# Performance work log

Measured on AMD Instinct MI355X. Metric: run time of the kernel, lower is better.

## Reference

```python
import jax, jax.numpy as jnp
import numpy as np

N, D_IN, D_P, N_HEADS, N_CTRS, D_OUT = 8192, 256, 64, 8, 128, 256


def setup_inputs() -> dict:
    key = jax.random.key(0)
    k = jax.random.split(key, 6)
    x = jax.random.normal(k[0], (N, D_IN), dtype=jnp.float32)
    ctrs = jax.random.normal(k[1], (N_HEADS, N_CTRS, D_P), dtype=jnp.float32) * 0.5
    Wv = jax.random.normal(k[2], (N_HEADS, N_CTRS, D_P, D_P), dtype=jnp.float32) * 0.02
    Ov = jax.random.normal(k[3], (N_HEADS, N_CTRS, D_P), dtype=jnp.float32) * 0.02
    Wq = jax.random.normal(k[4], (D_IN, D_P, N_HEADS), dtype=jnp.float32) * 0.05
    Wo = jax.random.normal(k[5], (N_HEADS * D_P, D_OUT), dtype=jnp.float32) * 0.02
    return {"x": x, "ctrs": ctrs, "Wv": Wv, "Ov": Ov, "Wq": Wq, "Wo": Wo}


def reference(x, ctrs, Wv, Ov, Wq, Wo):
    # project input per head: (N,d_in) x (d_in,d_p,h) -> (h,N,d_p)
    x_in = jnp.einsum('ni,iph->hnp', x, Wq)
    # RBF soft assignments over centroids: (h,N,c)
    dist_sq = jnp.sum((x_in[:, :, None, :] - ctrs[:, None, :, :]) ** 2, axis=-1)
    assignments = jax.nn.softmax(-dist_sq, axis=2)
    # soft-weighted per-cluster matrices: (h,N,g,p)
    scored_weights = jnp.einsum('hnc,hcgp->hngp', assignments, Wv)
    # soft-weighted offsets: (h,N,p)
    scored_offsets = jnp.einsum('hnc,hcp->hnp', assignments, Ov)
    # elementwise multiply (broadcast over g) then reduce over g, as in original
    heads_out = jnp.sum(scored_weights * x_in[:, :, None, :], axis=2) + scored_offsets
    # NOTE: original reshapes (h,N,p) directly into (N, h*p) in row-major order
    heads_out = heads_out.reshape(x.shape[0], N_HEADS * D_P)
    return heads_out @ Wo
```

## Files before the change

kernel.cpp:

```cpp
#include <hip/hip_runtime.h>
#include <math.h>

#define NROWS 8192
#define DIN   256
#define NH    8
#define NC    128
#define DOUT  256

typedef unsigned short ushort_t;
typedef __attribute__((ext_vector_type(8))) short bf16x8;
typedef __attribute__((ext_vector_type(4))) float f32x4;
typedef __attribute__((ext_vector_type(8))) unsigned short u16x8;

static __device__ __forceinline__ ushort_t f2bf(float f) {
  union { float f; unsigned u; } v; v.f = f;
  unsigned r = v.u + 0x7fffu + ((v.u >> 16) & 1u);
  return (ushort_t)(r >> 16);
}
static __device__ __forceinline__ float bf2f(ushort_t h) {
  union { unsigned u; float f; } v; v.u = ((unsigned)h) << 16;
  return v.f;
}

#define MFMA16(a, b, c) __builtin_amdgcn_mfma_f32_16x16x32_bf16((a), (b), (c), 0, 0, 0)
#define GLOAD_LDS16(g, l)                                                     \
  __builtin_amdgcn_global_load_lds(                                           \
      (const __attribute__((address_space(1))) void*)(g),                     \
      (__attribute__((address_space(3))) void*)(l), 16, 0, 0)

__global__ __launch_bounds__(256) void prep_kernel(
    const float* __restrict__ Wq, const float* __restrict__ ctrs,
    const float* __restrict__ Wo, const float* __restrict__ Wv,
    const float* __restrict__ Ov, ushort_t* __restrict__ wcvtT,
    ushort_t* __restrict__ ctr3T, float* __restrict__ cbias,
    ushort_t* __restrict__ WoT, ushort_t* __restrict__ W2bT) {
  int bid = blockIdx.x;
  int t = threadIdx.x;
  if (bid < 512) {
    int j = bid, k = t;
    int h = j >> 6, p = j & 63;
    float v = Wq[((size_t)k * 64 + p) * 8 + h];
    ushort_t hi = f2bf(v), lo = f2bf(v - bf2f(hi));
    wcvtT[(size_t)j * 512 + k]       = hi;
    wcvtT[(size_t)j * 512 + 256 + k] = lo;
  } else if (bid < 768) {
    int idx = (bid - 512) * 4 + (t >> 6);
    int p = t & 63;
    float v = ctrs[(size_t)idx * 64 + p];
    float sq = v * v;
    #pragma unroll
    for (int off = 32; off >= 1; off >>= 1) sq += __shfl_xor(sq, off, 64);
    if (p == 0) cbias[idx] = -sq;
    ushort_t hi = f2bf(v), lo = f2bf(v - bf2f(hi));
    ctr3T[(size_t)idx * 192 + p]       = hi;
    ctr3T[(size_t)idx * 192 + 64 + p]  = lo;
    ctr3T[(size_t)idx * 192 + 128 + p] = hi;
  } else if (bid < 1280) {
    int k = bid - 768;
    int n = t;
    WoT[(size_t)n * 512 + k] = f2bf(Wo[(size_t)k * 256 + n]);
  } else {
    int b = (bid - 1280) * 4 + (t >> 6);
    int p = t & 63;
    int h = b >> 7, c = b & 127;
    const float* wv = Wv + (size_t)b * 4096;
    float acc = 0.f;
    #pragma unroll 16
    for (int g = 0; g < 64; ++g) acc += wv[g * 64 + p];
    W2bT[((size_t)h * 128 + p) * 128 + c]      = f2bf(acc);
    W2bT[((size_t)h * 128 + 64 + p) * 128 + c] = f2bf(Ov[(size_t)b * 64 + p]);
  }
}

__global__ __launch_bounds__(256) void gemm2_kernel(
    const ushort_t* __restrict__ A, const ushort_t* __restrict__ Bt,
    float* __restrict__ out) {
  __shared__ ushort_t At[32 * 64];
  __shared__ ushort_t Bl[64 * 64];
  const int t = threadIdx.x;
  const int w = t >> 6, l = t & 63;
  const int wr = w >> 1, wc = w & 1;
  const int m0 = (blockIdx.x >> 2) * 32, n0 = (blockIdx.x & 3) * 64;
  const int lr = l & 15, lk = l >> 4;

  f32x4 acc[2];
  #pragma unroll
  for (int b = 0; b < 2; ++b) acc[b] = (f32x4){0.f, 0.f, 0.f, 0.f};

  for (int k0 = 0; k0 < 512; k0 += 64) {
    {
      int q = w * 64 + l;
      int row = q >> 3, s = q & 7;
      int kl = k0 + ((s ^ (row & 7)) << 3);
      GLOAD_LDS16(A + (size_t)(m0 + row) * 512 + kl,
                  (char*)At + (size_t)w * 1024);
    }
    #pragma unroll
    for (int i = 0; i < 2; ++i) {
      int q = (i * 4 + w) * 64 + l;
      int row = q >> 3, s = q & 7;
      int kl = k0 + ((s ^ (row & 7)) << 3);
      GLOAD_LDS16(Bt + (size_t)(n0 + row) * 512 + kl,
                  (char*)Bl + (size_t)(i * 4 + w) * 1024);
    }
    __syncthreads();
    #pragma unroll
    for (int kk = 0; kk < 2; ++kk) {
      int rowa = wr * 16 + lr;
      int sa = (kk * 4 + lk) ^ (rowa & 7);
      bf16x8 af = *(const bf16x8*)((const char*)At + rowa * 128 + sa * 16);
      #pragma unroll
      for (int b = 0; b < 2; ++b) {
        int row = wc * 32 + b * 16 + lr;
        int s = (kk * 4 + lk) ^ (row & 7);
        bf16x8 bfr = *(const bf16x8*)((const char*)Bl + row * 128 + s * 16);
        acc[b] = MFMA16(af, bfr, acc[b]);
      }
    }
    __syncthreads();
  }
  #pragma unroll
  for (int b = 0; b < 2; ++b) {
    #pragma unroll
    for (int r = 0; r < 4; ++r) {
      int rowg = m0 + wr * 16 + lk * 4 + r;
      int colg = n0 + wc * 32 + b * 16 + lr;
      out[(size_t)rowg * 256 + colg] = acc[b][r];
    }
  }
}

__global__ __launch_bounds__(512, 4) void fused_pair_kernel(
    const float* __restrict__ x,
    const ushort_t* __restrict__ wcvtT,
    const ushort_t* __restrict__ ctr3T,
    const float* __restrict__ cbias,
    const ushort_t* __restrict__ W2bT,
    ushort_t* __restrict__ ho2) {
  __shared__ __align__(16) char Au_raw[36864];
  __shared__ char B0lds[16384];
  __shared__ char B1lds[16384];
  __shared__ float cb_lds[128];

  ushort_t* Axh = (ushort_t*)Au_raw;
  ushort_t* Axl = (ushort_t*)(Au_raw + 18432);
  ushort_t* A1  = (ushort_t*)Au_raw;
  ushort_t* A2  = (ushort_t*)Au_raw;

  const int t = threadIdx.x;
  const int w = t >> 6, l = t & 63;
  const int lr = l & 15, lk = l >> 4;
  const int h = blockIdx.x >> 6;
  const int n0 = (blockIdx.x & 63) * 128;

#define STAGE_B(BUF, SRC, LDB, KOFF)                                          \
  {                                                                           \
    _Pragma("unroll")                                                         \
    for (int i = 0; i < 2; ++i) {                                             \
      int q = (i * 8 + w) * 64 + l;                                           \
      int row = q >> 3, s = q & 7;                                            \
      GLOAD_LDS16((SRC) + (size_t)(h * 128 + row) * (LDB) + (KOFF) +          \
                      ((s ^ (row & 7)) << 3),                                 \
                  (char*)(BUF) + (size_t)(i * 8 + w) * 1024);                 \
    }                                                                         \
  }

#define STAGE_BX(BUF, KC)                                                     \
  {                                                                           \
    _Pragma("unroll")                                                         \
    for (int i = 0; i < 2; ++i) {                                             \
      int q = (i * 8 + w) * 64 + l;                                           \
      int row = q >> 3, s = q & 7;                                            \
      int sw = (s ^ (row & 7)) << 3;                                          \
      int jj = h * 64 + (row & 63);                                           \
      int koff = (row < 64 ? 0 : 256) + (KC) * 64 + sw;                       \
      GLOAD_LDS16(wcvtT + (size_t)jj * 512 + koff,                            \
                  (char*)(BUF) + (size_t)(i * 8 + w) * 1024);                 \
    }                                                                         \
  }

#define MFMA_STEP(BUF, ACC, KBASE, ASPLIT)                                    \
  {                                                                           \
    _Pragma("unroll")                                                         \
    for (int kk = 0; kk < 2; ++kk) {                                          \
      int klog = (KBASE) + kk * 32 + lk * 8;                                  \
      int kp = (ASPLIT) ? (klog < 64 ? klog : klog - 64) : klog;              \
      bf16x8 af = *(const bf16x8*)&A1[(w * 16 + lr) * 136 + kp];              \
      _Pragma("unroll")                                                       \
      for (int cj = 0; cj < 8; ++cj) {                                        \
        int brow = cj * 16 + lr;                                              \
        int slot = (kk * 4 + lk) ^ (brow & 7);                                \
        bf16x8 bfr =                                                          \
            *(const bf16x8*)((const char*)(BUF) + brow * 128 + slot * 16);    \
        (ACC)[cj] = MFMA16(af, bfr, (ACC)[cj]);                               \
      }                                                                       \
    }                                                                         \
  }

#define MFMAX(BUF)                                                            \
  {                                                                           \
    _Pragma("unroll")                                                         \
    for (int kk = 0; kk < 2; ++kk) {                                          \
      bf16x8 ah = *(const bf16x8*)&Axh[(w * 16 + lr) * 72 + kk * 32 + lk * 8];\
      bf16x8 al = *(const bf16x8*)&Axl[(w * 16 + lr) * 72 + kk * 32 + lk * 8];\
      _Pragma("unroll")                                                       \
      for (int cj = 0; cj < 4; ++cj) {                                        \
        int rh = cj * 16 + lr;                                                \
        int slot = (kk * 4 + lk) ^ (rh & 7);                                  \
        bf16x8 bh = *(const bf16x8*)((const char*)(BUF) + rh * 128 + slot * 16);\
        bf16x8 bl = *(const bf16x8*)((const char*)(BUF) + (64 + rh) * 128 + slot * 16);\
        acc_x[cj] = MFMA16(ah, bh, acc_x[cj]);                                \
        acc_x[cj] = MFMA16(al, bh, acc_x[cj]);                                \
        acc_x[cj] = MFMA16(ah, bl, acc_x[cj]);                                \
      }                                                                       \
    }                                                                         \
  }

#define BAR() __builtin_amdgcn_s_barrier()
#define SCHED() __builtin_amdgcn_sched_barrier(0)
#define WAITALL_BAR()                                                         \
  {                                                                           \
    asm volatile("s_waitcnt vmcnt(0) lgkmcnt(0)" ::: "memory");               \
    SCHED(); BAR(); SCHED();                                                  \
  }

  const int xrow = t >> 2;
  const int xseg = (t & 3) << 4;
  const float* xb = x + (size_t)(n0 + xrow) * 256 + xseg;
  float4 xr[4];

#define LOAD_X(KC)                                                            \
  {                                                                           \
    _Pragma("unroll")                                                         \
    for (int j = 0; j < 4; ++j) xr[j] = *(const float4*)(xb + (KC) * 64 + j * 4); \
  }

#define CVT_AX()                                                              \
  {                                                                           \
    u16x8 hv0, hv1, lv0, lv1;                                                 \
    _Pragma("unroll")                                                         \
    for (int j = 0; j < 2; ++j) {                                             \
      float f4[8] = {xr[j*2].x, xr[j*2].y, xr[j*2].z, xr[j*2].w,              \
                     xr[j*2+1].x, xr[j*2+1].y, xr[j*2+1].z, xr[j*2+1].w};     \
      _Pragma("unroll")                                                       \
      for (int e = 0; e < 8; ++e) {                                           \
        ushort_t hi = f2bf(f4[e]);                                            \
        if (j == 0) { hv0[e] = hi; lv0[e] = f2bf(f4[e] - bf2f(hi)); }         \
        else        { hv1[e] = hi; lv1[e] = f2bf(f4[e] - bf2f(hi)); }         \
      }                                                                       \
    }                                                                         \
    *(u16x8*)&Axh[xrow * 72 + xseg]     = hv0;                                \
    *(u16x8*)&Axh[xrow * 72 + xseg + 8] = hv1;                                \
    *(u16x8*)&Axl[xrow * 72 + xseg]     = lv0;                                \
    *(u16x8*)&Axl[xrow * 72 + xseg + 8] = lv1;                                \
  }

#define SOFTMAX(ACC)                                                          \
  {                                                                           \
    float cbv[8];                                                             \
    _Pragma("unroll")                                                         \
    for (int cj = 0; cj < 8; ++cj) cbv[cj] = cb_lds[cj * 16 + lr];            \
    _Pragma("unroll")                                                         \
    for (int r = 0; r < 4; ++r) {                                             \
      float v[8];                                                             \
      float m = -1e30f;                                                       \
      _Pragma("unroll")                                                       \
      for (int cj = 0; cj < 8; ++cj) {                                        \
        v[cj] = 2.f * (ACC)[cj][r] + cbv[cj];                                 \
        m = fmaxf(m, v[cj]);                                                  \
      }                                                                       \
      m = fmaxf(m, __shfl_xor(m, 1, 64));                                     \
      m = fmaxf(m, __shfl_xor(m, 2, 64));                                     \
      m = fmaxf(m, __shfl_xor(m, 4, 64));                                     \
      m = fmaxf(m, __shfl_xor(m, 8, 64));                                     \
      float s = 0.f;                                                          \
      _Pragma("unroll")                                                       \
      for (int cj = 0; cj < 8; ++cj) {                                        \
        v[cj] = __expf(v[cj] - m);                                            \
        s += v[cj];                                                           \
      }                                                                       \
      s += __shfl_xor(s, 1, 64);                                              \
      s += __shfl_xor(s, 2, 64);                                              \
      s += __shfl_xor(s, 4, 64);                                              \
      s += __shfl_xor(s, 8, 64);                                              \
      float inv = 1.f / s;                                                    \
      int row = w * 16 + lk * 4 + r;                                          \
      _Pragma("unroll")                                                       \
      for (int cj = 0; cj < 8; ++cj)                                          \
        A2[row * 136 + cj * 16 + lr] = f2bf(v[cj] * inv);                     \
    }                                                                         \
  }

  cb_lds[t & 127] = cbias[h * 128 + (t & 127)];
  STAGE_BX(B0lds, 0);
  LOAD_X(0);
  f32x4 acc_x[4];
  #pragma unroll
  for (int cj = 0; cj < 4; ++cj) acc_x[cj] = (f32x4){0.f, 0.f, 0.f, 0.f};
  CVT_AX();
  WAITALL_BAR();

  STAGE_BX(B1lds, 1);
  LOAD_X(1);
  MFMAX(B0lds);
  CVT_AX();
  WAITALL_BAR();
  STAGE_BX(B0lds, 2);
  LOAD_X(2);
  MFMAX(B1lds);
  CVT_AX();
  WAITALL_BAR();
  STAGE_BX(B1lds, 3);
  LOAD_X(3);
  MFMAX(B0lds);
  CVT_AX();
  WAITALL_BAR();
  STAGE_B(B0lds, ctr3T, 192, 0);
  MFMAX(B1lds);
  WAITALL_BAR();

  STAGE_B(B1lds, ctr3T, 192, 64);
  #pragma unroll
  for (int cj = 0; cj < 4; ++cj) {
    #pragma unroll
    for (int r = 0; r < 4; ++r) {
      int row = w * 16 + lk * 4 + r;
      int p = cj * 16 + lr;
      float v0 = acc_x[cj][r];
      ushort_t hi0 = f2bf(v0);
      A1[row * 136 + p] = hi0;
      A1[row * 136 + 64 + p] = f2bf(v0 - bf2f(hi0));
    }
  }
  f32x4 acc[8];
  #pragma unroll
  for (int cj = 0; cj < 8; ++cj) acc[cj] = (f32x4){0.f, 0.f, 0.f, 0.f};
  MFMA_STEP(B0lds, acc, 0, 1);
  WAITALL_BAR();
  STAGE_B(B0lds, ctr3T, 192, 128);
  MFMA_STEP(B1lds, acc, 64, 1);
  WAITALL_BAR();
  STAGE_B(B1lds, W2bT, 128, 0);
  MFMA_STEP(B0lds, acc, 128, 1);
  WAITALL_BAR();
  STAGE_B(B0lds, W2bT, 128, 64);
  SOFTMAX(acc);
  f32x4 accT[8];
  #pragma unroll
  for (int cj = 0; cj < 8; ++cj) accT[cj] = (f32x4){0.f, 0.f, 0.f, 0.f};
  MFMA_STEP(B1lds, accT, 0, 0);
  WAITALL_BAR();
  MFMA_STEP(B0lds, accT, 64, 0);
  #pragma unroll
  for (int cj = 0; cj < 4; ++cj) {
    #pragma unroll
    for (int r = 0; r < 4; ++r) {
      int row = w * 16 + lk * 4 + r;
      int p = cj * 16 + lr;
      float hov = acc_x[cj][r] * accT[cj][r] + accT[cj + 4][r];
      ((ushort_t*)B1lds)[row * 64 + p] = f2bf(hov);
    }
  }
  asm volatile("s_waitcnt lgkmcnt(0)" ::: "memory");
  SCHED(); BAR(); SCHED();
  #pragma unroll
  for (int i = 0; i < 2; ++i) {
    int q = i * 512 + t;
    int row = q >> 3, s = q & 7;
    uint4 v = *(const uint4*)((const char*)B1lds + row * 128 + s * 16);
    *(uint4*)(ho2 + ((size_t)h * NROWS + n0 + row) * 64 + s * 8) = v;
  }
#undef STAGE_B
#undef STAGE_BX
#undef MFMA_STEP
#undef MFMAX
#undef BAR
#undef SCHED
#undef WAITALL_BAR
#undef LOAD_X
#undef CVT_AX
#undef SOFTMAX
}

extern "C" void kernel_launch(void* const* d_in, const int* in_sizes, int n_in,
                              void* d_out, int out_size, void* d_ws, size_t ws_size,
                              hipStream_t stream) {
  (void)in_sizes; (void)n_in; (void)out_size; (void)ws_size;
  const float* x    = (const float*)d_in[0];
  const float* ctrs = (const float*)d_in[1];
  const float* Wv   = (const float*)d_in[2];
  const float* Ov   = (const float*)d_in[3];
  const float* Wq   = (const float*)d_in[4];
  const float* Wo   = (const float*)d_in[5];
  float* out = (float*)d_out;

  char* wsb = (char*)d_ws;
  ushort_t* wcvtT = (ushort_t*)wsb;
  ushort_t* ctr3T = (ushort_t*)(wsb + 524288);
  float*    cb    = (float*)   (wsb + 917504);
  ushort_t* W2bT  = (ushort_t*)(wsb + 921600);
  ushort_t* WoT   = (ushort_t*)(wsb + 1183744);
  ushort_t* ho2   = (ushort_t*)(wsb + 2097152);

  prep_kernel<<<1536, 256, 0, stream>>>(Wq, ctrs, Wo, Wv, Ov,
                                        wcvtT, ctr3T, cb, WoT, W2bT);
  fused_pair_kernel<<<512, 512, 0, stream>>>(x, wcvtT, ctr3T, cb, W2bT, ho2);
  gemm2_kernel<<<1024, 256, 0, stream>>>(ho2, WoT, out);
}
```

Measured before the change: 39.86 us.

## Replace split-bf16 emulation with single fp16 MFMA for projection and distance GEMMs

The x·Wq projection and the x_in·ctrs distance GEMM used to emulate higher precision with bf16 hi/lo splits, costing three MFMAs per product and doubling staged bytes. Both now use a single fp16 MFMA on fp16-converted operands. The K-loop is restaged in 128-wide chunks, which removes two pipeline stages and their barriers. Prep writes smaller fp16 workspaces. The trade-off is lower accuracy in the softmax logits, where fp16 rounding of x and of the projected features gets amplified, and overflow is possible if values exceed the fp16 range.

```diff
diff --git a/kernel.cpp b/kernel.cpp
--- a/kernel.cpp
+++ b/kernel.cpp
@@ -9,8 +9,8 @@
 
 typedef unsigned short ushort_t;
 typedef __attribute__((ext_vector_type(8))) short bf16x8;
+typedef __attribute__((ext_vector_type(8))) _Float16 f16x8;
 typedef __attribute__((ext_vector_type(4))) float f32x4;
-typedef __attribute__((ext_vector_type(8))) unsigned short u16x8;
 
 static __device__ __forceinline__ ushort_t f2bf(float f) {
   union { float f; unsigned u; } v; v.f = f;
@@ -23,6 +23,7 @@
 }
 
 #define MFMA16(a, b, c) __builtin_amdgcn_mfma_f32_16x16x32_bf16((a), (b), (c), 0, 0, 0)
+#define MFMA16F(a, b, c) __builtin_amdgcn_mfma_f32_16x16x32_f16((a), (b), (c), 0, 0, 0)
 #define GLOAD_LDS16(g, l)                                                     \
   __builtin_amdgcn_global_load_lds(                                           \
       (const __attribute__((address_space(1))) void*)(g),                     \
@@ -31,8 +32,8 @@
 __global__ __launch_bounds__(256) void prep_kernel(
     const float* __restrict__ Wq, const float* __restrict__ ctrs,
     const float* __restrict__ Wo, const float* __restrict__ Wv,
-    const float* __restrict__ Ov, ushort_t* __restrict__ wcvtT,
-    ushort_t* __restrict__ ctr3T, float* __restrict__ cbias,
+    const float* __restrict__ Ov, _Float16* __restrict__ wq16,
+    _Float16* __restrict__ ctr16, float* __restrict__ cbias,
     ushort_t* __restrict__ WoT, ushort_t* __restrict__ W2bT) {
   int bid = blockIdx.x;
   int t = threadIdx.x;
@@ -40,9 +41,7 @@
     int j = bid, k = t;
     int h = j >> 6, p = j & 63;
     float v = Wq[((size_t)k * 64 + p) * 8 + h];
-    ushort_t hi = f2bf(v), lo = f2bf(v - bf2f(hi));
-    wcvtT[(size_t)j * 512 + k]       = hi;
-    wcvtT[(size_t)j * 512 + 256 + k] = lo;
+    wq16[(size_t)j * 256 + k] = (_Float16)v;
   } else if (bid < 768) {
     int idx = (bid - 512) * 4 + (t >> 6);
     int p = t & 63;
@@ -51,10 +50,7 @@
     #pragma unroll
     for (int off = 32; off >= 1; off >>= 1) sq += __shfl_xor(sq, off, 64);
     if (p == 0) cbias[idx] = -sq;
-    ushort_t hi = f2bf(v), lo = f2bf(v - bf2f(hi));
-    ctr3T[(size_t)idx * 192 + p]       = hi;
-    ctr3T[(size_t)idx * 192 + 64 + p]  = lo;
-    ctr3T[(size_t)idx * 192 + 128 + p] = hi;
+    ctr16[(size_t)idx * 64 + p] = (_Float16)v;
   } else if (bid < 1280) {
     int k = bid - 768;
     int n = t;
@@ -132,19 +128,18 @@
 
 __global__ __launch_bounds__(512, 4) void fused_pair_kernel(
     const float* __restrict__ x,
-    const ushort_t* __restrict__ wcvtT,
-    const ushort_t* __restrict__ ctr3T,
+    const _Float16* __restrict__ wq16,
+    const _Float16* __restrict__ ctr16,
     const float* __restrict__ cbias,
     const ushort_t* __restrict__ W2bT,
     ushort_t* __restrict__ ho2) {
-  __shared__ __align__(16) char Au_raw[36864];
+  __shared__ __align__(16) char Au_raw[34816];
   __shared__ char B0lds[16384];
   __shared__ char B1lds[16384];
   __shared__ float cb_lds[128];
 
-  ushort_t* Axh = (ushort_t*)Au_raw;
-  ushort_t* Axl = (ushort_t*)(Au_raw + 18432);
-  ushort_t* A1  = (ushort_t*)Au_raw;
+  _Float16* Axf = (_Float16*)Au_raw;
+  _Float16* A1f = (_Float16*)Au_raw;
   ushort_t* A2  = (ushort_t*)Au_raw;
 
   const int t = threadIdx.x;
@@ -153,39 +148,73 @@
   const int h = blockIdx.x >> 6;
   const int n0 = (blockIdx.x & 63) * 128;
 
-#define STAGE_B(BUF, SRC, LDB, KOFF)                                          \
+#define STAGE_WQ2(BUF, KC2)                                                   \
   {                                                                           \
     _Pragma("unroll")                                                         \
     for (int i = 0; i < 2; ++i) {                                             \
-      int q = (i * 8 + w) * 64 + l;                                           \
+      int q = (i * 8 + w) * 64 + l;                              \
+      int jrow = q >> 4, s16 = q & 15;                                        \
+      int c2 = s16 >> 3, s = s16 & 7;                                         \
+      GLOAD_LDS16(wq16 + (size_t)(h * 64 + jrow) * 256 + (KC2) * 128 +        \
+                      c2 * 64 + ((s ^ (jrow & 7)) << 3),                      \
+                  (char*)(BUF) + (size_t)q * 16);                             \
+    }                                                                         \
+  }
+
+#define STAGE_B128(BUF, SRC, LDB, KOFF)                                       \
+  {                                                                           \
+    _Pragma("unroll")                                                         \
+    for (int i = 0; i < 2; ++i) {                                             \
+      int q = (i * 8 + w) * 64 + l;                              \
       int row = q >> 3, s = q & 7;                                            \
       GLOAD_LDS16((SRC) + (size_t)(h * 128 + row) * (LDB) + (KOFF) +          \
                       ((s ^ (row & 7)) << 3),                                 \
-                  (char*)(BUF) + (size_t)(i * 8 + w) * 1024);                 \
-    }                                                                         \
-  }
-
-#define STAGE_BX(BUF, KC)                                                     \
-  {                                                                           \
-    _Pragma("unroll")                                                         \
-    for (int i = 0; i < 2; ++i) {                                             \
-      int q = (i * 8 + w) * 64 + l;                                           \
-      int row = q >> 3, s = q & 7;                                            \
-      int sw = (s ^ (row & 7)) << 3;                                          \
-      int jj = h * 64 + (row & 63);                                           \
-      int koff = (row < 64 ? 0 : 256) + (KC) * 64 + sw;                       \
-      GLOAD_LDS16(wcvtT + (size_t)jj * 512 + koff,                            \
-                  (char*)(BUF) + (size_t)(i * 8 + w) * 1024);                 \
-    }                                                                         \
-  }
-
-#define MFMA_STEP(BUF, ACC, KBASE, ASPLIT)                                    \
+                  (char*)(BUF) + (size_t)q * 16);                             \
+    }                                                                         \
+  }
+
+#define MFMAX(BUF)                                                            \
+  {                                                                           \
+    _Pragma("unroll")                                                         \
+    for (int c2 = 0; c2 < 2; ++c2) {                                          \
+      _Pragma("unroll")                                                       \
+      for (int kk = 0; kk < 2; ++kk) {                                        \
+        f16x8 af = *(const f16x8*)&Axf[(w * 16 + lr) * 136 + c2 * 64 +        \
+                                       kk * 32 + lk * 8];                     \
+        _Pragma("unroll")                                                     \
+        for (int cj = 0; cj < 4; ++cj) {                                      \
+          int rh = cj * 16 + lr;                                              \
+          int slot = (kk * 4 + lk) ^ (rh & 7);                                \
+          f16x8 bfr = *(const f16x8*)((const char*)(BUF) + rh * 256 +         \
+                                      c2 * 128 + slot * 16);                  \
+          acc_x[cj] = MFMA16F(af, bfr, acc_x[cj]);                            \
+        }                                                                     \
+      }                                                                       \
+    }                                                                         \
+  }
+
+#define MFMA_L(BUF, ACC)                                                      \
   {                                                                           \
     _Pragma("unroll")                                                         \
     for (int kk = 0; kk < 2; ++kk) {                                          \
-      int klog = (KBASE) + kk * 32 + lk * 8;                                  \
-      int kp = (ASPLIT) ? (klog < 64 ? klog : klog - 64) : klog;              \
-      bf16x8 af = *(const bf16x8*)&A1[(w * 16 + lr) * 136 + kp];              \
+      f16x8 af = *(const f16x8*)&A1f[(w * 16 + lr) * 136 + kk * 32 + lk * 8]; \
+      _Pragma("unroll")                                                       \
+      for (int cj = 0; cj < 8; ++cj) {                                        \
+        int brow = cj * 16 + lr;                                              \
+        int slot = (kk * 4 + lk) ^ (brow & 7);                                \
+        f16x8 bfr =                                                           \
+            *(const f16x8*)((const char*)(BUF) + brow * 128 + slot * 16);     \
+        (ACC)[cj] = MFMA16F(af, bfr, (ACC)[cj]);                              \
+      }                                                                       \
+    }                                                                         \
+  }
+
+#define MFMA_T(BUF, ACC, KB)                                                  \
+  {                                                                           \
+    _Pragma("unroll")                                                         \
+    for (int kk = 0; kk < 2; ++kk) {                                          \
+      bf16x8 af = *(const bf16x8*)&A2[(w * 16 + lr) * 136 + (KB) + kk * 32 +  \
+                                      lk * 8];                                \
       _Pragma("unroll")                                                       \
       for (int cj = 0; cj < 8; ++cj) {                                        \
         int brow = cj * 16 + lr;                                              \
@@ -197,25 +226,6 @@
     }                                                                         \
   }
 
-#define MFMAX(BUF)                                                            \
-  {                                                                           \
-    _Pragma("unroll")                                                         \
-    for (int kk = 0; kk < 2; ++kk) {                                          \
-      bf16x8 ah = *(const bf16x8*)&Axh[(w * 16 + lr) * 72 + kk * 32 + lk * 8];\
-      bf16x8 al = *(const bf16x8*)&Axl[(w * 16 + lr) * 72 + kk * 32 + lk * 8];\
-      _Pragma("unroll")                                                       \
-      for (int cj = 0; cj < 4; ++cj) {                                        \
-        int rh = cj * 16 + lr;                                                \
-        int slot = (kk * 4 + lk) ^ (rh & 7);                                  \
-        bf16x8 bh = *(const bf16x8*)((const char*)(BUF) + rh * 128 + slot * 16);\
-        bf16x8 bl = *(const bf16x8*)((const char*)(BUF) + (64 + rh) * 128 + slot * 16);\
-        acc_x[cj] = MFMA16(ah, bh, acc_x[cj]);                                \
-        acc_x[cj] = MFMA16(al, bh, acc_x[cj]);                                \
-        acc_x[cj] = MFMA16(ah, bl, acc_x[cj]);                                \
-      }                                                                       \
-    }                                                                         \
-  }
-
 #define BAR() __builtin_amdgcn_s_barrier()
 #define SCHED() __builtin_amdgcn_sched_barrier(0)
 #define WAITALL_BAR()                                                         \
@@ -225,132 +235,109 @@
   }
 
   const int xrow = t >> 2;
-  const int xseg = (t & 3) << 4;
-  const float* xb = x + (size_t)(n0 + xrow) * 256 + xseg;
-  float4 xr[4];
-
-#define LOAD_X(KC)                                                            \
-  {                                                                           \
-    _Pragma("unroll")                                                         \
-    for (int j = 0; j < 4; ++j) xr[j] = *(const float4*)(xb + (KC) * 64 + j * 4); \
-  }
-
-#define CVT_AX()                                                              \
-  {                                                                           \
-    u16x8 hv0, hv1, lv0, lv1;                                                 \
-    _Pragma("unroll")                                                         \
-    for (int j = 0; j < 2; ++j) {                                             \
-      float f4[8] = {xr[j*2].x, xr[j*2].y, xr[j*2].z, xr[j*2].w,              \
-                     xr[j*2+1].x, xr[j*2+1].y, xr[j*2+1].z, xr[j*2+1].w};     \
-      _Pragma("unroll")                                                       \
-      for (int e = 0; e < 8; ++e) {                                           \
-        ushort_t hi = f2bf(f4[e]);                                            \
-        if (j == 0) { hv0[e] = hi; lv0[e] = f2bf(f4[e] - bf2f(hi)); }         \
-        else        { hv1[e] = hi; lv1[e] = f2bf(f4[e] - bf2f(hi)); }         \
-      }                                                                       \
-    }                                                                         \
-    *(u16x8*)&Axh[xrow * 72 + xseg]     = hv0;                                \
-    *(u16x8*)&Axh[xrow * 72 + xseg + 8] = hv1;                                \
-    *(u16x8*)&Axl[xrow * 72 + xseg]     = lv0;                                \
-    *(u16x8*)&Axl[xrow * 72 + xseg + 8] = lv1;                                \
-  }
-
-#define SOFTMAX(ACC)                                                          \
-  {                                                                           \
-    float cbv[8];                                                             \
-    _Pragma("unroll")                                                         \
-    for (int cj = 0; cj < 8; ++cj) cbv[cj] = cb_lds[cj * 16 + lr];            \
-    _Pragma("unroll")                                                         \
-    for (int r = 0; r < 4; ++r) {                                             \
-      float v[8];                                                             \
-      float m = -1e30f;                                                       \
-      _Pragma("unroll")                                                       \
-      for (int cj = 0; cj < 8; ++cj) {                                        \
-        v[cj] = 2.f * (ACC)[cj][r] + cbv[cj];                                 \
-        m = fmaxf(m, v[cj]);                                                  \
-      }                                                                       \
-      m = fmaxf(m, __shfl_xor(m, 1, 64));                                     \
-      m = fmaxf(m, __shfl_xor(m, 2, 64));                                     \
-      m = fmaxf(m, __shfl_xor(m, 4, 64));                                     \
-      m = fmaxf(m, __shfl_xor(m, 8, 64));                                     \
-      float s = 0.f;                                                          \
-      _Pragma("unroll")                                                       \
-      for (int cj = 0; cj < 8; ++cj) {                                        \
-        v[cj] = __expf(v[cj] - m);                                            \
-        s += v[cj];                                                           \
-      }                                                                       \
-      s += __shfl_xor(s, 1, 64);                                              \
-      s += __shfl_xor(s, 2, 64);                                              \
-      s += __shfl_xor(s, 4, 64);                                              \
-      s += __shfl_xor(s, 8, 64);                                              \
-      float inv = 1.f / s;                                                    \
-      int row = w * 16 + lk * 4 + r;                                          \
-      _Pragma("unroll")                                                       \
-      for (int cj = 0; cj < 8; ++cj)                                          \
-        A2[row * 136 + cj * 16 + lr] = f2bf(v[cj] * inv);                     \
+  const int xsegf = (t & 3) << 4;
+  const float* xb = x + (size_t)(n0 + xrow) * 256 + xsegf;
+  float4 xr[8];
+
+#define LOAD_X2(KC2)                                                          \
+  {                                                                           \
+    _Pragma("unroll")                                                         \
+    for (int c2 = 0; c2 < 2; ++c2)                                            \
+      _Pragma("unroll")                                                       \
+      for (int j = 0; j < 4; ++j)                                             \
+        xr[c2 * 4 + j] =                                                      \
+            *(const float4*)(xb + (KC2) * 128 + c2 * 64 + j * 4);             \
+  }
+
+#define CVT_AX2()                                                             \
+  {                                                                           \
+    _Pragma("unroll")                                                         \
+    for (int c2 = 0; c2 < 2; ++c2) {                                          \
+      f16x8 h0, h1;                                                           \
+      float f0[8] = {xr[c2*4].x,   xr[c2*4].y,   xr[c2*4].z,   xr[c2*4].w,    \
+                     xr[c2*4+1].x, xr[c2*4+1].y, xr[c2*4+1].z, xr[c2*4+1].w}; \
+      float f1[8] = {xr[c2*4+2].x, xr[c2*4+2].y, xr[c2*4+2].z, xr[c2*4+2].w,  \
+                     xr[c2*4+3].x, xr[c2*4+3].y, xr[c2*4+3].z, xr[c2*4+3].w}; \
+      _Pragma("unroll")                                                       \
+      for (int e = 0; e < 8; ++e) { h0[e] = (_Float16)f0[e];                  \
+                                    h1[e] = (_Float16)f1[e]; }                \
+      *(f16x8*)&Axf[xrow * 136 + c2 * 64 + xsegf]     = h0;                   \
+      *(f16x8*)&Axf[xrow * 136 + c2 * 64 + xsegf + 8] = h1;                   \
     }                                                                         \
   }
 
   cb_lds[t & 127] = cbias[h * 128 + (t & 127)];
-  STAGE_BX(B0lds, 0);
-  LOAD_X(0);
+  STAGE_WQ2(B0lds, 0);
+  LOAD_X2(0);
   f32x4 acc_x[4];
   #pragma unroll
   for (int cj = 0; cj < 4; ++cj) acc_x[cj] = (f32x4){0.f, 0.f, 0.f, 0.f};
-  CVT_AX();
-  WAITALL_BAR();
-
-  STAGE_BX(B1lds, 1);
-  LOAD_X(1);
+  CVT_AX2();
+  WAITALL_BAR();
+
+  STAGE_WQ2(B1lds, 1);
+  LOAD_X2(1);
   MFMAX(B0lds);
-  CVT_AX();
-  WAITALL_BAR();
-  STAGE_BX(B0lds, 2);
-  LOAD_X(2);
+  CVT_AX2();
+  WAITALL_BAR();
+  STAGE_B128(B0lds, ctr16, 64, 0);
   MFMAX(B1lds);
-  CVT_AX();
-  WAITALL_BAR();
-  STAGE_BX(B1lds, 3);
-  LOAD_X(3);
-  MFMAX(B0lds);
-  CVT_AX();
-  WAITALL_BAR();
-  STAGE_B(B0lds, ctr3T, 192, 0);
-  MFMAX(B1lds);
-  WAITALL_BAR();
-
-  STAGE_B(B1lds, ctr3T, 192, 64);
   #pragma unroll
   for (int cj = 0; cj < 4; ++cj) {
     #pragma unroll
     for (int r = 0; r < 4; ++r) {
       int row = w * 16 + lk * 4 + r;
-      int p = cj * 16 + lr;
-      float v0 = acc_x[cj][r];
-      ushort_t hi0 = f2bf(v0);
-      A1[row * 136 + p] = hi0;
-      A1[row * 136 + 64 + p] = f2bf(v0 - bf2f(hi0));
-    }
-  }
+      A1f[row * 136 + cj * 16 + lr] = (_Float16)acc_x[cj][r];
+    }
+  }
+  WAITALL_BAR();
+  STAGE_B128(B1lds, W2bT, 128, 0);
   f32x4 acc[8];
   #pragma unroll
   for (int cj = 0; cj < 8; ++cj) acc[cj] = (f32x4){0.f, 0.f, 0.f, 0.f};
-  MFMA_STEP(B0lds, acc, 0, 1);
-  WAITALL_BAR();
-  STAGE_B(B0lds, ctr3T, 192, 128);
-  MFMA_STEP(B1lds, acc, 64, 1);
-  WAITALL_BAR();
-  STAGE_B(B1lds, W2bT, 128, 0);
-  MFMA_STEP(B0lds, acc, 128, 1);
-  WAITALL_BAR();
-  STAGE_B(B0lds, W2bT, 128, 64);
-  SOFTMAX(acc);
+  MFMA_L(B0lds, acc);
+  {
+    float cbv[8];
+    #pragma unroll
+    for (int cj = 0; cj < 8; ++cj) cbv[cj] = cb_lds[cj * 16 + lr];
+    #pragma unroll
+    for (int r = 0; r < 4; ++r) {
+      float v[8];
+      float m = -1e30f;
+      #pragma unroll
+      for (int cj = 0; cj < 8; ++cj) {
+        v[cj] = 2.f * acc[cj][r] + cbv[cj];
+        m = fmaxf(m, v[cj]);
+      }
+      m = fmaxf(m, __shfl_xor(m, 1, 64));
+      m = fmaxf(m, __shfl_xor(m, 2, 64));
+      m = fmaxf(m, __shfl_xor(m, 4, 64));
+      m = fmaxf(m, __shfl_xor(m, 8, 64));
+      float s = 0.f;
+      #pragma unroll
+      for (int cj = 0; cj < 8; ++cj) {
+        v[cj] = __expf(v[cj] - m);
+        s += v[cj];
+      }
+      s += __shfl_xor(s, 1, 64);
+      s += __shfl_xor(s, 2, 64);
+      s += __shfl_xor(s, 4, 64);
+      s += __shfl_xor(s, 8, 64);
+      float inv = 1.f / s;
+      int row = w * 16 + lk * 4 + r;
+      #pragma unroll
+      for (int cj = 0; cj < 8; ++cj)
+        A2[row * 136 + cj * 16 + lr] = f2bf(v[cj] * inv);
+    }
+  }
+  WAITALL_BAR();
+  STAGE_B128(B0lds, W2bT, 128, 64);
   f32x4 accT[8];
   #pragma unroll
   for (int cj = 0; cj < 8; ++cj) accT[cj] = (f32x4){0.f, 0.f, 0.f, 0.f};
-  MFMA_STEP(B1lds, accT, 0, 0);
-  WAITALL_BAR();
-  MFMA_STEP(B0lds, accT, 64, 0);
+  MFMA_T(B1lds, accT, 0);
+  WAITALL_BAR();
+  MFMA_T(B0lds, accT, 64);
   #pragma unroll
   for (int cj = 0; cj < 4; ++cj) {
     #pragma unroll
@@ -370,16 +357,16 @@
     uint4 v = *(const uint4*)((const char*)B1lds + row * 128 + s * 16);
     *(uint4*)(ho2 + ((size_t)h * NROWS + n0 + row) * 64 + s * 8) = v;
   }
-#undef STAGE_B
-#undef STAGE_BX
-#undef MFMA_STEP
+#undef STAGE_WQ2
+#undef STAGE_B128
 #undef MFMAX
+#undef MFMA_L
+#undef MFMA_T
 #undef BAR
 #undef SCHED
 #undef WAITALL_BAR
-#undef LOAD_X
-#undef CVT_AX
-#undef SOFTMAX
+#undef LOAD_X2
+#undef CVT_AX2
 }
 
 extern "C" void kernel_launch(void* const* d_in, const int* in_sizes, int n_in,
@@ -395,15 +382,15 @@
   float* out = (float*)d_out;
 
   char* wsb = (char*)d_ws;
-  ushort_t* wcvtT = (ushort_t*)wsb;
-  ushort_t* ctr3T = (ushort_t*)(wsb + 524288);
-  float*    cb    = (float*)   (wsb + 917504);
-  ushort_t* W2bT  = (ushort_t*)(wsb + 921600);
-  ushort_t* WoT   = (ushort_t*)(wsb + 1183744);
+  _Float16* wq16  = (_Float16*)wsb;
+  _Float16* ctr16 = (_Float16*)(wsb + 262144);
+  float*    cb    = (float*)   (wsb + 393216);
+  ushort_t* W2bT  = (ushort_t*)(wsb + 397312);
+  ushort_t* WoT   = (ushort_t*)(wsb + 659456);
   ushort_t* ho2   = (ushort_t*)(wsb + 2097152);
 
   prep_kernel<<<1536, 256, 0, stream>>>(Wq, ctrs, Wo, Wv, Ov,
-                                        wcvtT, ctr3T, cb, WoT, W2bT);
-  fused_pair_kernel<<<512, 512, 0, stream>>>(x, wcvtT, ctr3T, cb, W2bT, ho2);
+                                        wq16, ctr16, cb, WoT, W2bT);
+  fused_pair_kernel<<<512, 512, 0, stream>>>(x, wq16, ctr16, cb, W2bT, ho2);
   gemm2_kernel<<<1024, 256, 0, stream>>>(ho2, WoT, out);
 }
```

New measurement: 35.15 us (median of 2 runs). 1.13x faster.
